# Optimization experiments

Measured on AMD Instinct MI355X. Metric: run time of the kernel, lower is better.

Reference implementation:

```python
import jax, jax.numpy as jnp
import numpy as np

N_NODES = 100000
N_EDGES = 1600000


def gcn_conv(x, edge_index, W, b):
    """PyG-style GCNConv: self-loops + symmetric normalization + scatter-add."""
    n = x.shape[0]
    src, dst = edge_index[0], edge_index[1]
    loop = jnp.arange(n, dtype=src.dtype)
    src = jnp.concatenate([src, loop])
    dst = jnp.concatenate([dst, loop])
    h = x @ W  # [n, out] transform before propagate (PyG order)
    deg = jax.ops.segment_sum(jnp.ones_like(dst, dtype=h.dtype), dst, num_segments=n)
    dinv = jnp.where(deg > 0, deg ** -0.5, 0.0)
    norm = dinv[src] * dinv[dst]  # [E+n]
    msgs = h[src] * norm[:, None]  # gather + scale (largest intermediate)
    out = jax.ops.segment_sum(msgs, dst, num_segments=n)
    return out + b


def setup_inputs() -> dict:
    key = jax.random.key(0)
    ks = jax.random.split(key, 8)
    edge_attr = jax.random.normal(ks[0], (N_NODES, 5), dtype=jnp.float32)
    edge_index = jax.random.randint(ks[1], (2, N_EDGES), 0, N_NODES, dtype=jnp.int64)
    def lin(k, fan_in, fan_out):
        bound = 1.0 / np.sqrt(fan_in)
        return jax.random.uniform(k, (fan_in, fan_out), jnp.float32, -bound, bound)
    return {
        "edge_attr": edge_attr,
        "edge_index": edge_index,
        "W1": lin(ks[2], 5, 64),
        "b1": jnp.zeros((64,), jnp.float32),
        "W2": lin(ks[3], 64, 32),
        "b2": jnp.zeros((32,), jnp.float32),
        "fcW1": lin(ks[4], 32, 16),
        "fcb1": jnp.zeros((16,), jnp.float32),
        "fcW2": lin(ks[5], 16, 2),
        "fcb2": jnp.zeros((2,), jnp.float32),
    }


def reference(edge_attr, edge_index, W1, b1, W2, b2, fcW1, fcb1, fcW2, fcb2):
    x = jax.nn.relu(gcn_conv(edge_attr, edge_index, W1, b1))
    x = jax.nn.relu(gcn_conv(x, edge_index, W2, b2))
    x = jax.nn.relu(x @ fcW1 + fcb1)
    return x @ fcW2 + fcb2
```

## Files before the change

kernel.cpp:

```cpp
#include <hip/hip_runtime.h>


#define MS_TILE 2048
#define MAXB 512
#define AGG_NODES 32
#define AGG_STAGE 1024

__global__ __launch_bounds__(256) void histA(const int* __restrict__ dst,
                                             int* __restrict__ histG, int E) {
    __shared__ int h[MAXB];
    int t = threadIdx.x;
    h[t] = 0;
    h[t + 256] = 0;
    __syncthreads();
    int base = blockIdx.x * MS_TILE;
    int cnt = min(MS_TILE, E - base);
    for (int k = t; k < cnt; k += 256) atomicAdd(&h[dst[base + k] >> 8], 1);
    __syncthreads();
    histG[blockIdx.x * MAXB + t] = h[t];
    histG[blockIdx.x * MAXB + 256 + t] = h[t + 256];
}

__global__ __launch_bounds__(256) void scanTiles(const int* __restrict__ histG,
                                                 int* __restrict__ offsG,
                                                 int* __restrict__ bucketTotal,
                                                 int nTiles) {
    __shared__ int scn[256];
    int b = blockIdx.x, t = threadIdx.x;
    int run = 0;
    for (int base = 0; base < nTiles; base += 256) {
        int idx = base + t;
        int v = (idx < nTiles) ? histG[idx * MAXB + b] : 0;
        scn[t] = v;
        __syncthreads();
        int incl = v;
        for (int d = 1; d < 256; d <<= 1) {
            int add = (t >= d) ? scn[t - d] : 0;
            __syncthreads();
            incl += add;
            scn[t] = incl;
            __syncthreads();
        }
        if (idx < nTiles) offsG[idx * MAXB + b] = incl - v + run;
        run += scn[255];
        __syncthreads();
    }
    if (t == 0) bucketTotal[b] = run;
}

__global__ __launch_bounds__(256) void multisplit2(
    const int* __restrict__ src, const int* __restrict__ dst,
    const int* __restrict__ histG, const int* __restrict__ offsG,
    const int* __restrict__ btot, int* __restrict__ gbaseOut,
    unsigned* __restrict__ binned, int E) {
    __shared__ unsigned stage[MS_TILE];
    __shared__ unsigned short sb[MS_TILE];
    __shared__ int hoff[MAXB + 1];
    __shared__ int hcur[MAXB];
    __shared__ int gb[MAXB];
    __shared__ int scn[256];
    int t = threadIdx.x;
    int tile = blockIdx.x;
    int base = tile * MS_TILE;
    int cnt = min(MS_TILE, E - base);

    int b0 = btot[2 * t], b1v = btot[2 * t + 1];
    int s2 = b0 + b1v;
    scn[t] = s2;
    __syncthreads();
    int incl2 = s2;
    for (int d = 1; d < 256; d <<= 1) {
        int add = (t >= d) ? scn[t - d] : 0;
        __syncthreads();
        incl2 += add;
        scn[t] = incl2;
        __syncthreads();
    }
    int ex2 = incl2 - s2;
    gb[2 * t] = ex2 + offsG[tile * MAXB + 2 * t];
    gb[2 * t + 1] = ex2 + b0 + offsG[tile * MAXB + 2 * t + 1];
    if (tile == 0) {
        gbaseOut[2 * t] = ex2;
        gbaseOut[2 * t + 1] = ex2 + b0;
        if (t == 255) gbaseOut[MAXB] = E;
    }

    int a0 = histG[tile * MAXB + 2 * t];
    int a1 = histG[tile * MAXB + 2 * t + 1];
    int s = a0 + a1;
    scn[t] = s;
    __syncthreads();
    int incl = s;
    for (int d = 1; d < 256; d <<= 1) {
        int add = (t >= d) ? scn[t - d] : 0;
        __syncthreads();
        incl += add;
        scn[t] = incl;
        __syncthreads();
    }
    int ex = incl - s;
    hoff[2 * t] = ex;
    hoff[2 * t + 1] = ex + a0;
    hcur[2 * t] = ex;
    hcur[2 * t + 1] = ex + a0;
    if (t == 255) hoff[MAXB] = cnt;
    __syncthreads();
    for (int k = t; k < cnt; k += 256) {
        int d = dst[base + k];
        int b = d >> 8;
        int p = atomicAdd(&hcur[b], 1);
        stage[p] = ((unsigned)src[base + k] << 8) | (unsigned)(d & 255);
        sb[p] = (unsigned short)b;
    }
    __syncthreads();
    for (int k = t; k < cnt; k += 256) {
        int b = sb[k];
        binned[gb[b] + (k - hoff[b])] = stage[k];
    }
}

__global__ __launch_bounds__(256) void place_fine2(
    const unsigned* __restrict__ binned, const int* __restrict__ gbase,
    const float* __restrict__ x, int* __restrict__ offs, int* __restrict__ deg,
    float* __restrict__ dinv, float* __restrict__ y, int* __restrict__ srcs, int n) {
    __shared__ int cnt[256];
    __shared__ int scn[256];
    __shared__ int lcur[256];
    int t = threadIdx.x, b = blockIdx.x;
    int node0 = b << 8;
    int nn = min(256, n - node0);
    int e0 = gbase[b], e1 = gbase[b + 1];
    cnt[t] = 0;
    __syncthreads();
    for (int k = e0 + t; k < e1; k += 256) atomicAdd(&cnt[binned[k] & 255u], 1);
    __syncthreads();
    int c = cnt[t];
    scn[t] = c;
    __syncthreads();
    int incl = c;
    for (int d = 1; d < 256; d <<= 1) {
        int add = (t >= d) ? scn[t - d] : 0;
        __syncthreads();
        incl += add;
        scn[t] = incl;
        __syncthreads();
    }
    int myoff = e0 + (incl - c);
    lcur[t] = myoff;
    if (t < nn) {
        int node = node0 + t;
        offs[node] = myoff;
        deg[node] = c;
        float di = 1.0f / sqrtf((float)(c + 1));
        dinv[node] = di;
        const float* xr = x + (size_t)node * 5;
        float4 a = {xr[0] * di, xr[1] * di, xr[2] * di, xr[3] * di};
        float4 bq = {xr[4] * di, 0.f, 0.f, 0.f};
        *(float4*)(y + (size_t)node * 8) = a;
        *(float4*)(y + (size_t)node * 8 + 4) = bq;
    }
    __syncthreads();
    for (int k = e0 + t; k < e1; k += 256) {
        unsigned w = binned[k];
        int p = atomicAdd(&lcur[w & 255u], 1);
        srcs[p] = (int)(w >> 8);
    }
}

__global__ __launch_bounds__(128) void agg_xin(
    const float* __restrict__ y, const int* __restrict__ srcs,
    const int* __restrict__ offs, const int* __restrict__ deg,
    const float* __restrict__ dinv, float* __restrict__ z, int n) {
    int i = blockIdx.x * 128 + threadIdx.x;
    if (i >= n) return;
    const float4* yv = (const float4*)y;
    float4 a = yv[(size_t)i * 2];
    float4 b = yv[(size_t)i * 2 + 1];
    int off = offs[i], cnt = deg[i];
    int p = 0;
    for (; p + 4 <= cnt; p += 4) {
        int s0 = srcs[off + p], s1 = srcs[off + p + 1];
        int s2 = srcs[off + p + 2], s3 = srcs[off + p + 3];
        float4 v0 = yv[(size_t)s0 * 2];
        float4 w0 = yv[(size_t)s0 * 2 + 1];
        float4 v1 = yv[(size_t)s1 * 2];
        float4 w1 = yv[(size_t)s1 * 2 + 1];
        float4 v2 = yv[(size_t)s2 * 2];
        float4 w2 = yv[(size_t)s2 * 2 + 1];
        float4 v3 = yv[(size_t)s3 * 2];
        float4 w3 = yv[(size_t)s3 * 2 + 1];
        a.x += (v0.x + v1.x) + (v2.x + v3.x);
        a.y += (v0.y + v1.y) + (v2.y + v3.y);
        a.z += (v0.z + v1.z) + (v2.z + v3.z);
        a.w += (v0.w + v1.w) + (v2.w + v3.w);
        b.x += (w0.x + w1.x) + (w2.x + w3.x);
    }
    for (; p < cnt; ++p) {
        int s0 = srcs[off + p];
        float4 v0 = yv[(size_t)s0 * 2];
        float w0 = y[(size_t)s0 * 8 + 4];
        a.x += v0.x; a.y += v0.y; a.z += v0.z; a.w += v0.w;
        b.x += w0;
    }
    float di = dinv[i];
    float4 oa = {a.x * di, a.y * di, a.z * di, a.w * di};
    float4 ob = {b.x * di, 0.f, 0.f, 0.f};
    float4* zv = (float4*)z;
    zv[(size_t)i * 2] = oa;
    zv[(size_t)i * 2 + 1] = ob;
}

__global__ __launch_bounds__(256) void transform12(
    const float* __restrict__ z, const float* __restrict__ W1,
    const float* __restrict__ b1, const float* __restrict__ W2,
    const float* __restrict__ dinv, float* __restrict__ h2, int n) {
    __shared__ float w1s[320];
    __shared__ float b1s[64];
    __shared__ float w2s[64 * 32];
    __shared__ float o1[32 * 64];
    int t = threadIdx.x;
    w1s[t] = W1[t];
    if (t < 64) {
        w1s[t + 256] = W1[t + 256];
        b1s[t] = b1[t];
    }
#pragma unroll
    for (int r = 0; r < 8; ++r) w2s[r * 256 + t] = W2[r * 256 + t];
    __syncthreads();
    int node0 = blockIdx.x * 32;
#pragma unroll
    for (int r = 0; r < 8; ++r) {
        int idx = r * 256 + t;
        int li = idx >> 6, f = idx & 63;
        int i = node0 + li;
        if (i < n) {
            const float* zr = z + (size_t)i * 8;
            float acc = b1s[f];
#pragma unroll
            for (int k = 0; k < 5; ++k) acc += zr[k] * w1s[k * 64 + f];
            o1[li * 64 + f] = fmaxf(acc, 0.0f);
        }
    }
    __syncthreads();
#pragma unroll
    for (int r = 0; r < 4; ++r) {
        int idx = r * 256 + t;
        int li = idx >> 5, g = idx & 31;
        int i = node0 + li;
        if (i < n) {
            float acc = 0.f;
#pragma unroll
            for (int k = 0; k < 64; ++k) acc += o1[li * 64 + k] * w2s[k * 32 + g];
            h2[(size_t)i * 32 + g] = acc * dinv[i];
        }
    }
}

__global__ __launch_bounds__(256) void agg2_fc(
    const float* __restrict__ h, const int* __restrict__ srcs,
    const int* __restrict__ offs, const int* __restrict__ deg,
    const float* __restrict__ dinv, const float* __restrict__ b2,
    const float* __restrict__ fcW1, const float* __restrict__ fcb1,
    const float* __restrict__ fcW2, const float* __restrict__ fcb2,
    float* __restrict__ out, int n, int E) {
    __shared__ int sidx[AGG_STAGE];
    __shared__ float sm[AGG_NODES * 33];
    __shared__ float x3s[AGG_NODES * 16];
    __shared__ float w1s[512];
    __shared__ float w2s[32];
    __shared__ float b1s[16];
    __shared__ float b2s[2];
    __shared__ float bs2[32];
    int t = threadIdx.x;
    w1s[t] = fcW1[t];
    w1s[t + 256] = fcW1[t + 256];
    if (t < 32) { w2s[t] = fcW2[t]; bs2[t] = b2[t]; }
    if (t < 16) b1s[t] = fcb1[t];
    if (t < 2) b2s[t] = fcb2[t];

    int node0 = blockIdx.x * AGG_NODES;
    int li = t >> 3, fq = t & 7;
    int i = node0 + li;
    bool live = (i < n);
    const char* hb = (const char*)h;

    int e0 = offs[node0];
    int eEnd = (node0 + AGG_NODES < n) ? offs[node0 + AGG_NODES] : E;
    int myOff = 0, myCnt = 0;
    float4 acc = {0.f, 0.f, 0.f, 0.f};
    if (live) {
        myOff = offs[i];
        myCnt = deg[i];
        acc = *(const float4*)(hb + ((size_t)i << 7) + (fq << 4));
    }

    for (int cs = e0; cs < eEnd; cs += AGG_STAGE) {
        int ce = min(cs + AGG_STAGE, eEnd);
        for (int k = cs + t; k < ce; k += 256) sidx[k - cs] = srcs[k] << 7;
        __syncthreads();
        int ps = max(myOff, cs), pe = min(myOff + myCnt, ce);
        int p = ps;
        for (; p + 8 <= pe; p += 8) {
            int o[8];
#pragma unroll
            for (int u = 0; u < 8; ++u) o[u] = sidx[p + u - cs];
            float4 v[8];
#pragma unroll
            for (int u = 0; u < 8; ++u)
                v[u] = *(const float4*)(hb + o[u] + (fq << 4));
#pragma unroll
            for (int u = 0; u < 8; ++u) {
                acc.x += v[u].x; acc.y += v[u].y;
                acc.z += v[u].z; acc.w += v[u].w;
            }
        }
        for (; p + 4 <= pe; p += 4) {
            int o0 = sidx[p - cs], o1 = sidx[p + 1 - cs];
            int o2 = sidx[p + 2 - cs], o3 = sidx[p + 3 - cs];
            float4 v0 = *(const float4*)(hb + o0 + (fq << 4));
            float4 v1 = *(const float4*)(hb + o1 + (fq << 4));
            float4 v2 = *(const float4*)(hb + o2 + (fq << 4));
            float4 v3 = *(const float4*)(hb + o3 + (fq << 4));
            acc.x += (v0.x + v1.x) + (v2.x + v3.x);
            acc.y += (v0.y + v1.y) + (v2.y + v3.y);
            acc.z += (v0.z + v1.z) + (v2.z + v3.z);
            acc.w += (v0.w + v1.w) + (v2.w + v3.w);
        }
        for (; p < pe; ++p) {
            float4 v = *(const float4*)(hb + sidx[p - cs] + (fq << 4));
            acc.x += v.x; acc.y += v.y; acc.z += v.z; acc.w += v.w;
        }
        __syncthreads();
    }

    if (live) {
        float di = dinv[i];
        int f0 = fq << 2;
        sm[li * 33 + f0 + 0] = fmaxf(di * acc.x + bs2[f0 + 0], 0.f);
        sm[li * 33 + f0 + 1] = fmaxf(di * acc.y + bs2[f0 + 1], 0.f);
        sm[li * 33 + f0 + 2] = fmaxf(di * acc.z + bs2[f0 + 2], 0.f);
        sm[li * 33 + f0 + 3] = fmaxf(di * acc.w + bs2[f0 + 3], 0.f);
    }
    __syncthreads();
#pragma unroll
    for (int r = 0; r < 2; ++r) {
        int idx = r * 256 + t;
        int lj = idx >> 4, j = idx & 15;
        if (node0 + lj < n) {
            float a = b1s[j];
#pragma unroll
            for (int k = 0; k < 32; ++k) a += sm[lj * 33 + k] * w1s[k * 16 + j];
            x3s[lj * 16 + j] = fmaxf(a, 0.f);
        }
    }
    __syncthreads();
    if (t < 64) {
        int lj = t >> 1, o = t & 1;
        if (node0 + lj < n) {
            float a = b2s[o];
#pragma unroll
            for (int j = 0; j < 16; ++j) a += x3s[lj * 16 + j] * w2s[j * 2 + o];
            out[(size_t)(node0 + lj) * 2 + o] = a;
        }
    }
}

extern "C" void kernel_launch(void* const* d_in, const int* in_sizes, int n_in,
                              void* d_out, int out_size, void* d_ws, size_t ws_size,
                              hipStream_t stream) {
    const float* edge_attr = (const float*)d_in[0];
    const int* edge_index  = (const int*)d_in[1];
    const float* W1   = (const float*)d_in[2];
    const float* b1   = (const float*)d_in[3];
    const float* W2   = (const float*)d_in[4];
    const float* b2   = (const float*)d_in[5];
    const float* fcW1 = (const float*)d_in[6];
    const float* fcb1 = (const float*)d_in[7];
    const float* fcW2 = (const float*)d_in[8];
    const float* fcb2 = (const float*)d_in[9];
    float* out = (float*)d_out;

    int n = in_sizes[0] / 5;
    int E = in_sizes[1] / 2;
    int NBkt = (n + 255) >> 8;
    int nTiles = (E + MS_TILE - 1) / MS_TILE;
    const int* src = edge_index;
    const int* dst = edge_index + E;

    char* ws = (char*)d_ws;
    auto alloc = [&](size_t bytes) {
        char* p = ws;
        ws += (bytes + 255) & ~(size_t)255;
        return p;
    };
    int*      deg    = (int*)alloc((size_t)n * 4);
    int*      offs   = (int*)alloc((size_t)n * 4);
    float*    dinv   = (float*)alloc((size_t)n * 4);
    int*      histG  = (int*)alloc((size_t)nTiles * MAXB * 4);
    int*      offsG  = (int*)alloc((size_t)nTiles * MAXB * 4);
    int*      btot   = (int*)alloc((size_t)MAXB * 4);
    int*      gbase  = (int*)alloc((size_t)(MAXB + 1) * 4);
    int*      srcs   = (int*)alloc((size_t)E * 4);
    unsigned* binned = (unsigned*)alloc((size_t)E * 4);
    float*    y      = (float*)alloc((size_t)n * 8 * 4);
    float*    z      = (float*)alloc((size_t)n * 8 * 4);
    float*    h2     = (float*)alloc((size_t)n * 32 * 4);

    histA<<<nTiles, 256, 0, stream>>>(dst, histG, E);
    scanTiles<<<MAXB, 256, 0, stream>>>(histG, offsG, btot, nTiles);
    multisplit2<<<nTiles, 256, 0, stream>>>(src, dst, histG, offsG, btot, gbase,
                                            binned, E);
    place_fine2<<<NBkt, 256, 0, stream>>>(binned, gbase, edge_attr, offs, deg, dinv,
                                          y, srcs, n);
    agg_xin<<<(n + 127) / 128, 128, 0, stream>>>(y, srcs, offs, deg, dinv, z, n);
    transform12<<<(n + 31) / 32, 256, 0, stream>>>(z, W1, b1, W2, dinv, h2, n);
    agg2_fc<<<(n + AGG_NODES - 1) / AGG_NODES, 256, 0, stream>>>(
        h2, srcs, offs, deg, dinv, b2, fcW1, fcb1, fcW2, fcb2, out, n, E);
}
```

Before: 198.9 us.

## Replace CSR fine placement with per-bucket LDS atomic aggregation over coarse bins

Drops the fine per-node sort (prefix scan and srcs scatter) and the offs/deg arrays. Both aggregation layers now walk the coarse 256-node bucketed edge list with 1024-thread blocks and accumulate into shared memory with float atomics. This saves a full pass that writes and reads srcs. In exchange, all neighbour sums go through LDS atomics, which can contend on hot nodes, and there are only about 391 blocks of 1024 threads to fill the GPU.

```diff
diff --git a/kernel.cpp b/kernel.cpp
--- a/kernel.cpp
+++ b/kernel.cpp
@@ -3,8 +3,6 @@
 
 #define MS_TILE 2048
 #define MAXB 512
-#define AGG_NODES 32
-#define AGG_STAGE 1024
 
 __global__ __launch_bounds__(256) void histA(const int* __restrict__ dst,
                                              int* __restrict__ histG, int E) {
@@ -119,13 +117,11 @@
     }
 }
 
-__global__ __launch_bounds__(256) void place_fine2(
+__global__ __launch_bounds__(256) void prep(
     const unsigned* __restrict__ binned, const int* __restrict__ gbase,
-    const float* __restrict__ x, int* __restrict__ offs, int* __restrict__ deg,
-    float* __restrict__ dinv, float* __restrict__ y, int* __restrict__ srcs, int n) {
+    const float* __restrict__ x, float* __restrict__ dinv,
+    float* __restrict__ y, int n) {
     __shared__ int cnt[256];
-    __shared__ int scn[256];
-    __shared__ int lcur[256];
     int t = threadIdx.x, b = blockIdx.x;
     int node0 = b << 8;
     int nn = min(256, n - node0);
@@ -134,24 +130,9 @@
     __syncthreads();
     for (int k = e0 + t; k < e1; k += 256) atomicAdd(&cnt[binned[k] & 255u], 1);
     __syncthreads();
-    int c = cnt[t];
-    scn[t] = c;
-    __syncthreads();
-    int incl = c;
-    for (int d = 1; d < 256; d <<= 1) {
-        int add = (t >= d) ? scn[t - d] : 0;
-        __syncthreads();
-        incl += add;
-        scn[t] = incl;
-        __syncthreads();
-    }
-    int myoff = e0 + (incl - c);
-    lcur[t] = myoff;
     if (t < nn) {
         int node = node0 + t;
-        offs[node] = myoff;
-        deg[node] = c;
-        float di = 1.0f / sqrtf((float)(c + 1));
+        float di = 1.0f / sqrtf((float)(cnt[t] + 1));
         dinv[node] = di;
         const float* xr = x + (size_t)node * 5;
         float4 a = {xr[0] * di, xr[1] * di, xr[2] * di, xr[3] * di};
@@ -159,55 +140,45 @@
         *(float4*)(y + (size_t)node * 8) = a;
         *(float4*)(y + (size_t)node * 8 + 4) = bq;
     }
-    __syncthreads();
-    for (int k = e0 + t; k < e1; k += 256) {
+}
+
+__global__ __launch_bounds__(1024) void aggL1(
+    const unsigned* __restrict__ binned, const int* __restrict__ gbase,
+    const float* __restrict__ y, const float* __restrict__ dinv,
+    float* __restrict__ z, int n) {
+    __shared__ float acc[256 * 9];
+    int t = threadIdx.x, b = blockIdx.x;
+    int node0 = b << 8;
+    for (int idx = t; idx < 256 * 9; idx += 1024) acc[idx] = 0.f;
+    __syncthreads();
+    int e0 = gbase[b], e1 = gbase[b + 1];
+    const float4* yv = (const float4*)y;
+    for (int k = e0 + t; k < e1; k += 1024) {
         unsigned w = binned[k];
-        int p = atomicAdd(&lcur[w & 255u], 1);
-        srcs[p] = (int)(w >> 8);
-    }
-}
-
-__global__ __launch_bounds__(128) void agg_xin(
-    const float* __restrict__ y, const int* __restrict__ srcs,
-    const int* __restrict__ offs, const int* __restrict__ deg,
-    const float* __restrict__ dinv, float* __restrict__ z, int n) {
-    int i = blockIdx.x * 128 + threadIdx.x;
-    if (i >= n) return;
-    const float4* yv = (const float4*)y;
-    float4 a = yv[(size_t)i * 2];
-    float4 b = yv[(size_t)i * 2 + 1];
-    int off = offs[i], cnt = deg[i];
-    int p = 0;
-    for (; p + 4 <= cnt; p += 4) {
-        int s0 = srcs[off + p], s1 = srcs[off + p + 1];
-        int s2 = srcs[off + p + 2], s3 = srcs[off + p + 3];
-        float4 v0 = yv[(size_t)s0 * 2];
-        float4 w0 = yv[(size_t)s0 * 2 + 1];
-        float4 v1 = yv[(size_t)s1 * 2];
-        float4 w1 = yv[(size_t)s1 * 2 + 1];
-        float4 v2 = yv[(size_t)s2 * 2];
-        float4 w2 = yv[(size_t)s2 * 2 + 1];
-        float4 v3 = yv[(size_t)s3 * 2];
-        float4 w3 = yv[(size_t)s3 * 2 + 1];
-        a.x += (v0.x + v1.x) + (v2.x + v3.x);
-        a.y += (v0.y + v1.y) + (v2.y + v3.y);
-        a.z += (v0.z + v1.z) + (v2.z + v3.z);
-        a.w += (v0.w + v1.w) + (v2.w + v3.w);
-        b.x += (w0.x + w1.x) + (w2.x + w3.x);
-    }
-    for (; p < cnt; ++p) {
-        int s0 = srcs[off + p];
-        float4 v0 = yv[(size_t)s0 * 2];
-        float w0 = y[(size_t)s0 * 8 + 4];
-        a.x += v0.x; a.y += v0.y; a.z += v0.z; a.w += v0.w;
-        b.x += w0;
-    }
-    float di = dinv[i];
-    float4 oa = {a.x * di, a.y * di, a.z * di, a.w * di};
-    float4 ob = {b.x * di, 0.f, 0.f, 0.f};
-    float4* zv = (float4*)z;
-    zv[(size_t)i * 2] = oa;
-    zv[(size_t)i * 2 + 1] = ob;
+        int dl = (int)(w & 255u);
+        int s = (int)(w >> 8);
+        float4 v0 = yv[(size_t)s * 2];
+        float v4 = y[(size_t)s * 8 + 4];
+        float* a = acc + dl * 9;
+        atomicAdd(a + 0, v0.x);
+        atomicAdd(a + 1, v0.y);
+        atomicAdd(a + 2, v0.z);
+        atomicAdd(a + 3, v0.w);
+        atomicAdd(a + 4, v4);
+    }
+    __syncthreads();
+    for (int idx = t; idx < 512; idx += 1024) {
+        int ln = idx >> 1, h = idx & 1;
+        int i = node0 + ln;
+        if (i < n) {
+            float di = dinv[i];
+            float4 ys = yv[(size_t)i * 2 + h];
+            const float* a = acc + ln * 9 + h * 4;
+            float4 o = {di * (ys.x + a[0]), di * (ys.y + a[1]),
+                        di * (ys.z + a[2]), di * (ys.w + a[3])};
+            ((float4*)z)[(size_t)i * 2 + h] = o;
+        }
+    }
 }
 
 __global__ __launch_bounds__(256) void transform12(
@@ -256,95 +227,56 @@
     }
 }
 
-__global__ __launch_bounds__(256) void agg2_fc(
-    const float* __restrict__ h, const int* __restrict__ srcs,
-    const int* __restrict__ offs, const int* __restrict__ deg,
-    const float* __restrict__ dinv, const float* __restrict__ b2,
-    const float* __restrict__ fcW1, const float* __restrict__ fcb1,
-    const float* __restrict__ fcW2, const float* __restrict__ fcb2,
-    float* __restrict__ out, int n, int E) {
-    __shared__ int sidx[AGG_STAGE];
-    __shared__ float sm[AGG_NODES * 33];
-    __shared__ float x3s[AGG_NODES * 16];
+__global__ __launch_bounds__(1024) void aggL2_fc(
+    const unsigned* __restrict__ binned, const int* __restrict__ gbase,
+    const float* __restrict__ h2, const float* __restrict__ dinv,
+    const float* __restrict__ b2, const float* __restrict__ fcW1,
+    const float* __restrict__ fcb1, const float* __restrict__ fcW2,
+    const float* __restrict__ fcb2, float* __restrict__ out, int n) {
+    __shared__ float sm[256 * 33];
+    __shared__ float x3s[256 * 16];
     __shared__ float w1s[512];
     __shared__ float w2s[32];
     __shared__ float b1s[16];
     __shared__ float b2s[2];
     __shared__ float bs2[32];
-    int t = threadIdx.x;
-    w1s[t] = fcW1[t];
-    w1s[t + 256] = fcW1[t + 256];
-    if (t < 32) { w2s[t] = fcW2[t]; bs2[t] = b2[t]; }
-    if (t < 16) b1s[t] = fcb1[t];
-    if (t < 2) b2s[t] = fcb2[t];
-
-    int node0 = blockIdx.x * AGG_NODES;
-    int li = t >> 3, fq = t & 7;
-    int i = node0 + li;
-    bool live = (i < n);
-    const char* hb = (const char*)h;
-
-    int e0 = offs[node0];
-    int eEnd = (node0 + AGG_NODES < n) ? offs[node0 + AGG_NODES] : E;
-    int myOff = 0, myCnt = 0;
-    float4 acc = {0.f, 0.f, 0.f, 0.f};
-    if (live) {
-        myOff = offs[i];
-        myCnt = deg[i];
-        acc = *(const float4*)(hb + ((size_t)i << 7) + (fq << 4));
-    }
-
-    for (int cs = e0; cs < eEnd; cs += AGG_STAGE) {
-        int ce = min(cs + AGG_STAGE, eEnd);
-        for (int k = cs + t; k < ce; k += 256) sidx[k - cs] = srcs[k] << 7;
-        __syncthreads();
-        int ps = max(myOff, cs), pe = min(myOff + myCnt, ce);
-        int p = ps;
-        for (; p + 8 <= pe; p += 8) {
-            int o[8];
-#pragma unroll
-            for (int u = 0; u < 8; ++u) o[u] = sidx[p + u - cs];
-            float4 v[8];
-#pragma unroll
-            for (int u = 0; u < 8; ++u)
-                v[u] = *(const float4*)(hb + o[u] + (fq << 4));
-#pragma unroll
-            for (int u = 0; u < 8; ++u) {
-                acc.x += v[u].x; acc.y += v[u].y;
-                acc.z += v[u].z; acc.w += v[u].w;
-            }
-        }
-        for (; p + 4 <= pe; p += 4) {
-            int o0 = sidx[p - cs], o1 = sidx[p + 1 - cs];
-            int o2 = sidx[p + 2 - cs], o3 = sidx[p + 3 - cs];
-            float4 v0 = *(const float4*)(hb + o0 + (fq << 4));
-            float4 v1 = *(const float4*)(hb + o1 + (fq << 4));
-            float4 v2 = *(const float4*)(hb + o2 + (fq << 4));
-            float4 v3 = *(const float4*)(hb + o3 + (fq << 4));
-            acc.x += (v0.x + v1.x) + (v2.x + v3.x);
-            acc.y += (v0.y + v1.y) + (v2.y + v3.y);
-            acc.z += (v0.z + v1.z) + (v2.z + v3.z);
-            acc.w += (v0.w + v1.w) + (v2.w + v3.w);
-        }
-        for (; p < pe; ++p) {
-            float4 v = *(const float4*)(hb + sidx[p - cs] + (fq << 4));
-            acc.x += v.x; acc.y += v.y; acc.z += v.z; acc.w += v.w;
-        }
-        __syncthreads();
-    }
-
-    if (live) {
-        float di = dinv[i];
-        int f0 = fq << 2;
-        sm[li * 33 + f0 + 0] = fmaxf(di * acc.x + bs2[f0 + 0], 0.f);
-        sm[li * 33 + f0 + 1] = fmaxf(di * acc.y + bs2[f0 + 1], 0.f);
-        sm[li * 33 + f0 + 2] = fmaxf(di * acc.z + bs2[f0 + 2], 0.f);
-        sm[li * 33 + f0 + 3] = fmaxf(di * acc.w + bs2[f0 + 3], 0.f);
-    }
-    __syncthreads();
-#pragma unroll
-    for (int r = 0; r < 2; ++r) {
-        int idx = r * 256 + t;
+    int t = threadIdx.x, b = blockIdx.x;
+    int node0 = b << 8;
+    if (t < 512) w1s[t] = fcW1[t];
+    else if (t < 544) w2s[t - 512] = fcW2[t - 512];
+    else if (t < 560) b1s[t - 544] = fcb1[t - 544];
+    else if (t < 562) b2s[t - 560] = fcb2[t - 560];
+    else if (t < 594) bs2[t - 562] = b2[t - 562];
+    for (int idx = t; idx < 256 * 33; idx += 1024) sm[idx] = 0.f;
+    __syncthreads();
+
+    int e0 = gbase[b], e1 = gbase[b + 1];
+    int g = t >> 3, l8 = t & 7;
+    const float4* h2v = (const float4*)h2;
+    for (int k = e0 + g; k < e1; k += 128) {
+        unsigned w = binned[k];
+        int dl = (int)(w & 255u);
+        int s = (int)(w >> 8);
+        float4 v = h2v[(size_t)s * 8 + l8];
+        float* a = sm + dl * 33 + l8 * 4;
+        atomicAdd(a + 0, v.x);
+        atomicAdd(a + 1, v.y);
+        atomicAdd(a + 2, v.z);
+        atomicAdd(a + 3, v.w);
+    }
+    __syncthreads();
+    for (int idx = t; idx < 256 * 32; idx += 1024) {
+        int ln = idx >> 5, f = idx & 31;
+        int i = node0 + ln;
+        if (i < n) {
+            float v = dinv[i] * (h2[(size_t)i * 32 + f] + sm[ln * 33 + f]) + bs2[f];
+            sm[ln * 33 + f] = fmaxf(v, 0.f);
+        }
+    }
+    __syncthreads();
+#pragma unroll
+    for (int r = 0; r < 4; ++r) {
+        int idx = r * 1024 + t;
         int lj = idx >> 4, j = idx & 15;
         if (node0 + lj < n) {
             float a = b1s[j];
@@ -354,7 +286,7 @@
         }
     }
     __syncthreads();
-    if (t < 64) {
+    if (t < 512) {
         int lj = t >> 1, o = t & 1;
         if (node0 + lj < n) {
             float a = b2s[o];
@@ -393,14 +325,11 @@
         ws += (bytes + 255) & ~(size_t)255;
         return p;
     };
-    int*      deg    = (int*)alloc((size_t)n * 4);
-    int*      offs   = (int*)alloc((size_t)n * 4);
     float*    dinv   = (float*)alloc((size_t)n * 4);
     int*      histG  = (int*)alloc((size_t)nTiles * MAXB * 4);
     int*      offsG  = (int*)alloc((size_t)nTiles * MAXB * 4);
     int*      btot   = (int*)alloc((size_t)MAXB * 4);
     int*      gbase  = (int*)alloc((size_t)(MAXB + 1) * 4);
-    int*      srcs   = (int*)alloc((size_t)E * 4);
     unsigned* binned = (unsigned*)alloc((size_t)E * 4);
     float*    y      = (float*)alloc((size_t)n * 8 * 4);
     float*    z      = (float*)alloc((size_t)n * 8 * 4);
@@ -410,10 +339,9 @@
     scanTiles<<<MAXB, 256, 0, stream>>>(histG, offsG, btot, nTiles);
     multisplit2<<<nTiles, 256, 0, stream>>>(src, dst, histG, offsG, btot, gbase,
                                             binned, E);
-    place_fine2<<<NBkt, 256, 0, stream>>>(binned, gbase, edge_attr, offs, deg, dinv,
-                                          y, srcs, n);
-    agg_xin<<<(n + 127) / 128, 128, 0, stream>>>(y, srcs, offs, deg, dinv, z, n);
+    prep<<<NBkt, 256, 0, stream>>>(binned, gbase, edge_attr, dinv, y, n);
+    aggL1<<<NBkt, 1024, 0, stream>>>(binned, gbase, y, dinv, z, n);
     transform12<<<(n + 31) / 32, 256, 0, stream>>>(z, W1, b1, W2, dinv, h2, n);
-    agg2_fc<<<(n + AGG_NODES - 1) / AGG_NODES, 256, 0, stream>>>(
-        h2, srcs, offs, deg, dinv, b2, fcW1, fcb1, fcW2, fcb2, out, n, E);
-}
+    aggL2_fc<<<NBkt, 1024, 0, stream>>>(binned, gbase, h2, dinv, b2,
+                                        fcW1, fcb1, fcW2, fcb2, out, n);
+}
```

Measured after the change: 546.7 us. +174.9%, slower.
